# Kernel tuning notes

Hardware: AMD Instinct MI355X
Metric: run time of the kernel (lower is better)

## Reference

```python
import jax, jax.numpy as jnp
import numpy as np
from jax import lax

LOG2PI = float(np.log(2.0 * np.pi))
N_K, N_T, N_C, N_D, N_SPK = 256, 128, 32, 10, 1000000

def _std_normal_logpdf(x):
    return -0.5 * (x * x + LOG2PI)

def _normal_logpdf(x, mu, log_sig):
    z = (x - mu) * jnp.exp(-log_sig)
    return -0.5 * (z * z + LOG2PI) - log_sig

def safe_log(x, minval=1e-10):
    return jnp.log(x + minval)

def setup_inputs() -> dict:
    key = jax.random.key(0)
    ks_ = jax.random.split(key, 8)
    s = jax.random.normal(ks_[0], (N_SPK, N_D), dtype=jnp.float32)
    y = jax.random.normal(ks_[1], (N_K, N_T), dtype=jnp.float32)
    ks = jax.random.randint(ks_[2], (N_SPK,), 0, N_K, dtype=jnp.int32)
    ts = jax.random.randint(ks_[3], (N_SPK,), 0, N_T, dtype=jnp.int32)
    means = jax.random.normal(ks_[4], (N_C, N_D), dtype=jnp.float32)
    A = jax.random.normal(ks_[5], (N_C, N_D, N_D), dtype=jnp.float32)
    covs = jnp.einsum('cij,ckj->cik', A, A) / N_D + jnp.eye(N_D, dtype=jnp.float32)
    b_mu = jax.random.normal(ks_[6], (N_C,), dtype=jnp.float32)
    b_log_sig = jax.random.normal(ks_[7], (N_C,), dtype=jnp.float32)
    beta_mu = jax.random.normal(jax.random.fold_in(key, 10), (N_C, N_T), dtype=jnp.float32)
    beta_log_sig = jax.random.normal(jax.random.fold_in(key, 11), (N_C, N_T), dtype=jnp.float32)
    return {"s": s, "y": y, "ks": ks, "ts": ts, "means": means, "covs": covs,
            "b_mu": b_mu, "b_log_sig": b_log_sig, "beta_mu": beta_mu, "beta_log_sig": beta_log_sig}

def _mvn_ll(s, means, covs):
    # ll[n, c] = MVN(means[c], covs[c]).log_prob(s[n]); loop over small n_c via lax.map
    L = jnp.linalg.cholesky(covs)                       # (c, d, d)
    logdet = 2.0 * jnp.sum(jnp.log(jnp.diagonal(L, axis1=1, axis2=2)), axis=1)  # (c,)
    d = s.shape[1]
    def comp(args):
        mu, Lc, ld = args
        diff = s - mu                                   # (n, d)
        z = jax.scipy.linalg.solve_triangular(Lc, diff.T, lower=True)  # (d, n)
        return -0.5 * (d * LOG2PI + ld + jnp.sum(z * z, axis=0))       # (n,)
    return lax.map(comp, (means, L, logdet)).T          # (n, c)

def reference(s, y, ks, ts, means, covs, b_mu, b_log_sig, beta_mu, beta_log_sig):
    # sampling=False path: use variational means
    b_sample, beta_sample = b_mu, beta_mu               # (c,), (c, t)
    # log_lambdas[k, c, t] = b[c] + beta[c, t] * y[k, t]
    log_lambdas = b_sample[None, :, None] + beta_sample[None, :, :] * y[:, None, :]
    log_pis = jax.nn.log_softmax(log_lambdas, axis=1)   # (k, c, t)
    ll = _mvn_ll(s, means, covs)                        # (n, c)
    logits = ll + log_pis[ks, :, ts]                    # per-spike gather -> (n, c)
    r = jax.nn.softmax(logits, axis=1)                  # responsibilities (n, c)
    log_prior = jnp.sum(_std_normal_logpdf(b_sample)) + jnp.sum(_std_normal_logpdf(beta_sample))
    log_q = jnp.sum(_normal_logpdf(b_sample, b_mu, b_log_sig)) + \
            jnp.sum(_normal_logpdf(beta_sample, beta_mu, beta_log_sig))
    elbo = log_prior - log_q
    elbo += jnp.sum(r * logits)
    elbo -= jnp.sum(r * safe_log(r))
    return elbo
```

## Files before the change

kernel.cpp:

```cpp
#include <hip/hip_runtime.h>
#include <hip/hip_bf16.h>
#include <math.h>

#define NK 256
#define NT 128
#define NC 32
#define ND 10
#define NSPK 1000000
#define LOG2PI 1.8378770664093453f
#define NCHUNK ((NSPK + 255) / 256)
#define GRID 1024

#define FSTR 36
#define LDS_DW (256 * FSTR)

typedef __attribute__((ext_vector_type(8))) short short8;
typedef __attribute__((ext_vector_type(4))) float floatx4;
typedef __attribute__((ext_vector_type(4))) int intx4;

union FragCvt { intx4 i; short8 s; };


__device__ inline unsigned pack_bf16(float a, float b) {
  __hip_bfloat16 ha = __float2bfloat16(a), hb = __float2bfloat16(b);
  unsigned short ua, ub;
  __builtin_memcpy(&ua, &ha, 2);
  __builtin_memcpy(&ub, &hb, 2);
  return (unsigned)ua | ((unsigned)ub << 16);
}

__global__ void prep_kernel(const float* __restrict__ y,
                            const float* __restrict__ means,
                            const float* __restrict__ covs,
                            const float* __restrict__ b_mu,
                            const float* __restrict__ b_ls,
                            const float* __restrict__ beta_mu,
                            const float* __restrict__ beta_ls,
                            int* __restrict__ wt,
                            float* __restrict__ cpack,
                            float* __restrict__ pisT,
                            double* __restrict__ acc,
                            unsigned int* __restrict__ counter) {
  int blk = blockIdx.x;
  int tid = threadIdx.x;

  if (blk == 0) {
    int c = tid;
    if (c >= NC) return;

    float M[ND][ND];
    #pragma unroll
    for (int i = 0; i < ND; ++i)
      #pragma unroll
      for (int j = 0; j < ND; ++j)
        M[i][j] = covs[c * ND * ND + i * ND + j];

    float logdet = 0.f;
    #pragma unroll
    for (int j = 0; j < ND; ++j) {
      float d = M[j][j];
      #pragma unroll
      for (int k = 0; k < ND; ++k) if (k < j) d -= M[j][k] * M[j][k];
      float sq = sqrtf(d);
      M[j][j] = sq;
      logdet += 2.f * __logf(sq);
      float inv = 1.f / sq;
      #pragma unroll
      for (int i = 0; i < ND; ++i) {
        if (i > j) {
          float s2 = M[i][j];
          #pragma unroll
          for (int k = 0; k < ND; ++k) if (k < j) s2 -= M[i][k] * M[j][k];
          M[i][j] = s2 * inv;
        }
      }
    }

    #pragma unroll
    for (int j = 0; j < ND; ++j) {
      M[j][j] = 1.f / M[j][j];
      #pragma unroll
      for (int i = 0; i < ND; ++i) {
        if (i > j) {
          float s2 = 0.f;
          #pragma unroll
          for (int k = 0; k < ND; ++k) if (k >= j && k < i) s2 += M[i][k] * M[k][j];
          M[i][j] = -s2 / M[i][i];
        }
      }
    }

    float pd[ND];
    #pragma unroll
    for (int i = 0; i < ND; ++i) {
      #pragma unroll
      for (int jj = 0; jj < ND; ++jj) {
        if (jj >= i) {
          float s2 = 0.f;
          #pragma unroll
          for (int k = 0; k < ND; ++k) if (k >= jj) s2 += M[k][i] * M[k][jj];
          if (jj > i) M[i][jj] = s2;
          else pd[i] = s2;
        }
      }
    }

    float mu[ND], q[ND];
    #pragma unroll
    for (int i = 0; i < ND; ++i) mu[i] = means[c * ND + i];
    float muPmu = 0.f;
    #pragma unroll
    for (int i = 0; i < ND; ++i) {
      float a2 = pd[i] * mu[i];
      #pragma unroll
      for (int j = 0; j < ND; ++j) {
        if (j < i) a2 += M[j][i] * mu[j];
        if (j > i) a2 += M[i][j] * mu[j];
      }
      q[i] = a2;
      muPmu += mu[i] * a2;
    }
    float cst = -0.5f * ((float)ND * LOG2PI + logdet + muPmu);

    float wv[64];
    int p = 0;
    #pragma unroll
    for (int i = 0; i < ND; ++i)
      #pragma unroll
      for (int j = 0; j < ND; ++j)
        if (j >= i && !(i == 9 && j == 9))
          wv[p++] = (i == j) ? -0.5f * pd[i] : -M[i][j];
    #pragma unroll
    for (int i = 0; i < ND; ++i) wv[54 + i] = q[i];

    #pragma unroll
    for (int j = 0; j < 32; ++j) {
      float a = wv[2 * j], b = wv[2 * j + 1];
      float ah = __bfloat162float(__float2bfloat16(a));
      float bh = __bfloat162float(__float2bfloat16(b));
      wt[c * 32 + j] = (int)pack_bf16(ah, bh);
      wt[(32 + c) * 32 + j] = (int)pack_bf16(a - ah, b - bh);
    }
    cpack[c] = cst;
    cpack[32 + c] = -0.5f * pd[9];

  } else if (blk == 1) {
    float local = 0.f;
    for (int i = tid; i < NC; i += 256)
      local += fmaf(-0.5f * b_mu[i], b_mu[i], b_ls[i]);
    for (int i = tid; i < NC * NT; i += 256)
      local += fmaf(-0.5f * beta_mu[i], beta_mu[i], beta_ls[i]);
    #pragma unroll
    for (int off = 32; off > 0; off >>= 1) local += __shfl_down(local, off);
    __shared__ float red[4];
    if ((tid & 63) == 0) red[tid >> 6] = local;
    __syncthreads();
    if (tid == 0) {
      acc[0] = (double)(red[0] + red[1] + red[2] + red[3]);
      counter[0] = 0u;
    }

  } else {
    int id = (blk - 2) * 256 + tid;
    int t = id & (NT - 1);
    float yv = y[id];
    float v[NC];
    float m = -1e30f;
    #pragma unroll
    for (int c = 0; c < NC; ++c) {
      v[c] = fmaf(beta_mu[c * NT + t], yv, b_mu[c]);
      m = fmaxf(m, v[c]);
    }
    float ssum = 0.f;
    #pragma unroll
    for (int c = 0; c < NC; ++c) ssum += __expf(v[c] - m);
    float lz = m + __logf(ssum);
    float* outp = pisT + (size_t)id * NC;
    #pragma unroll
    for (int c = 0; c < NC; ++c) outp[c] = v[c] - lz;
  }
}

__global__ __launch_bounds__(256, 4)
void spike_kernel(const float* __restrict__ s,
                  const int* __restrict__ ks,
                  const int* __restrict__ ts,
                  const int* __restrict__ wt,
                  const float* __restrict__ cpack,
                  const float* __restrict__ pisT,
                  double* __restrict__ acc,
                  unsigned int* __restrict__ counter,
                  float* __restrict__ out) {
  __shared__ int lds[LDS_DW];
  __shared__ float red[4];

  int tid = threadIdx.x;
  int wv_ = tid >> 6, L = tid & 63;
  int r = L & 15, q = L >> 4;

  FragCvt bf[2][2][2];
  #pragma unroll
  for (int h = 0; h < 2; ++h)
    #pragma unroll
    for (int nt = 0; nt < 2; ++nt)
      #pragma unroll
      for (int ks2 = 0; ks2 < 2; ++ks2)
        bf[h][nt][ks2].i =
            *(const intx4*)&wt[(h * 32 + nt * 16 + r) * 32 + ks2 * 16 + q * 4];

  float lse_sum = 0.f;

  for (int ci = blockIdx.x; ci < NCHUNK; ci += GRID) {
    int n = ci * 256 + tid;
    int nc = n < NSPK ? n : (NSPK - 1);

    const float2* srow = (const float2*)(s + (size_t)nc * ND);
    float sv[ND];
    #pragma unroll
    for (int i = 0; i < 5; ++i) {
      float2 v2 = srow[i];
      sv[2 * i] = v2.x;
      sv[2 * i + 1] = v2.y;
    }
    int kk_ = ks[nc], tt_ = ts[nc];

    float fv[64];
    {
      int p = 0;
      #pragma unroll
      for (int i = 0; i < ND; ++i)
        #pragma unroll
        for (int j = 0; j < ND; ++j)
          if (j >= i && !(i == 9 && j == 9)) fv[p++] = sv[i] * sv[j];
      #pragma unroll
      for (int i = 0; i < ND; ++i) fv[54 + i] = sv[i];
    }

    __syncthreads();
    {
      int rb = tid * FSTR;
      #pragma unroll
      for (int ch = 0; ch < 8; ++ch) {
        intx4 v;
        v.x = (int)pack_bf16(fv[8 * ch + 0], fv[8 * ch + 1]);
        v.y = (int)pack_bf16(fv[8 * ch + 2], fv[8 * ch + 3]);
        v.z = (int)pack_bf16(fv[8 * ch + 4], fv[8 * ch + 5]);
        v.w = (int)pack_bf16(fv[8 * ch + 6], fv[8 * ch + 7]);
        *(intx4*)&lds[rb + ch * 4] = v;
      }
    }
    __syncthreads();

    floatx4 accf[4][2];
    #pragma unroll
    for (int mt = 0; mt < 4; ++mt)
      #pragma unroll
      for (int nt = 0; nt < 2; ++nt)
        accf[mt][nt] = (floatx4){0.f, 0.f, 0.f, 0.f};

    #pragma unroll
    for (int mt = 0; mt < 4; ++mt) {
      #pragma unroll
      for (int ks2 = 0; ks2 < 2; ++ks2) {
        FragCvt a;
        a.i = *(const intx4*)&lds[(wv_ * 64 + mt * 16 + r) * FSTR + ks2 * 16 + q * 4];
        #pragma unroll
        for (int nt = 0; nt < 2; ++nt) {
          accf[mt][nt] = __builtin_amdgcn_mfma_f32_16x16x32_bf16(
              a.s, bf[0][nt][ks2].s, accf[mt][nt], 0, 0, 0);
          accf[mt][nt] = __builtin_amdgcn_mfma_f32_16x16x32_bf16(
              a.s, bf[1][nt][ks2].s, accf[mt][nt], 0, 0, 0);
        }
      }
    }

    const float4* lpp = (const float4*)(pisT + (size_t)(kk_ * NT + tt_) * NC);
    float4 lpv[8];
    #pragma unroll
    for (int i = 0; i < 8; ++i) lpv[i] = lpp[i];

    __syncthreads();

    #pragma unroll
    for (int mt = 0; mt < 4; ++mt)
      #pragma unroll
      for (int nt = 0; nt < 2; ++nt)
        #pragma unroll
        for (int rr = 0; rr < 4; ++rr) {
          int srow_ = wv_ * 64 + mt * 16 + q * 4 + rr;
          lds[srow_ * FSTR + nt * 16 + r] = __float_as_int(accf[mt][nt][rr]);
        }
    __syncthreads();

    {
      float lp[32];
      #pragma unroll
      for (int i = 0; i < 8; ++i) {
        lp[4 * i + 0] = lpv[i].x; lp[4 * i + 1] = lpv[i].y;
        lp[4 * i + 2] = lpv[i].z; lp[4 * i + 3] = lpv[i].w;
      }
      float s9sq = sv[9] * sv[9];
      int base = tid * FSTR;
      float lg[32];
      #pragma unroll
      for (int g = 0; g < 8; ++g) {
        intx4 lv = *(const intx4*)&lds[base + g * 4];
        lg[4 * g + 0] = __int_as_float(lv.x);
        lg[4 * g + 1] = __int_as_float(lv.y);
        lg[4 * g + 2] = __int_as_float(lv.z);
        lg[4 * g + 3] = __int_as_float(lv.w);
      }
      #pragma unroll
      for (int c = 0; c < 32; ++c)
        lg[c] += lp[c] + fmaf(cpack[32 + c], s9sq, cpack[c]);

      float m = lg[0];
      #pragma unroll
      for (int c = 1; c < 32; ++c) m = fmaxf(m, lg[c]);
      float ssum = 0.f;
      #pragma unroll
      for (int c = 0; c < 32; ++c) ssum += __expf(lg[c] - m);
      if (n < NSPK) lse_sum += m + __logf(ssum);
    }
  }

  #pragma unroll
  for (int off = 32; off > 0; off >>= 1) lse_sum += __shfl_down(lse_sum, off);
  if ((tid & 63) == 0) red[tid >> 6] = lse_sum;
  __syncthreads();
  if (tid == 0) {
    atomicAdd(acc, (double)(red[0] + red[1] + red[2] + red[3]));
    __threadfence();
    unsigned int old = atomicAdd(counter, 1u);
    if (old == GRID - 1) {
      __threadfence();
      double v = atomicAdd(acc, 0.0);
      out[0] = (float)v;
    }
  }
}

extern "C" void kernel_launch(void* const* d_in, const int* in_sizes, int n_in,
                              void* d_out, int out_size, void* d_ws, size_t ws_size,
                              hipStream_t stream) {
  const float* s       = (const float*)d_in[0];
  const float* y       = (const float*)d_in[1];
  const int*   ks      = (const int*)d_in[2];
  const int*   ts      = (const int*)d_in[3];
  const float* means   = (const float*)d_in[4];
  const float* covs    = (const float*)d_in[5];
  const float* b_mu    = (const float*)d_in[6];
  const float* b_ls    = (const float*)d_in[7];
  const float* beta_mu = (const float*)d_in[8];
  const float* beta_ls = (const float*)d_in[9];
  float* out = (float*)d_out;

  char* ws = (char*)d_ws;
  double* acc           = (double*)ws;
  unsigned int* counter = (unsigned int*)(ws + 8);
  float* cpack          = (float*)(ws + 64);
  int* wt               = (int*)(ws + 1024);
  float* pisT           = (float*)(ws + 16384);

  prep_kernel<<<2 + (NK * NT) / 256, 256, 0, stream>>>(
      y, means, covs, b_mu, b_ls, beta_mu, beta_ls, wt, cpack, pisT, acc, counter);
  spike_kernel<<<GRID, 256, 0, stream>>>(
      s, ks, ts, wt, cpack, pisT, acc, counter, out);
}
```

Baseline: 168.0 us.

## Prefetch next chunk, use dynamic atomic work queue, store log-pis in fp16

The fixed grid-stride loop becomes an atomic work queue, and the next chunk's spike features and gather index are prefetched during the current chunk's MFMA and softmax. The log-pi table is stored as fp16, halving the gather traffic, and feature packing streams into LDS in groups of eight instead of holding a 64-float array. This aims to hide global load latency and balance load across blocks. In exchange it lowers the precision of log_pis, holds more registers live, and adds an atomic per chunk.

```diff
diff --git a/kernel.cpp b/kernel.cpp
--- a/kernel.cpp
+++ b/kernel.cpp
@@ -1,5 +1,6 @@
 #include <hip/hip_runtime.h>
 #include <hip/hip_bf16.h>
+#include <hip/hip_fp16.h>
 #include <math.h>
 
 #define NK 256
@@ -19,6 +20,7 @@
 typedef __attribute__((ext_vector_type(4))) int intx4;
 
 union FragCvt { intx4 i; short8 s; };
+union H2Cvt { int i; __half2 h; };
 
 
 __device__ inline unsigned pack_bf16(float a, float b) {
@@ -38,9 +40,10 @@
                             const float* __restrict__ beta_ls,
                             int* __restrict__ wt,
                             float* __restrict__ cpack,
-                            float* __restrict__ pisT,
+                            __half* __restrict__ pisT,
                             double* __restrict__ acc,
-                            unsigned int* __restrict__ counter) {
+                            unsigned int* __restrict__ counter,
+                            unsigned int* __restrict__ queue) {
   int blk = blockIdx.x;
   int tid = threadIdx.x;
 
@@ -158,6 +161,7 @@
     if (tid == 0) {
       acc[0] = (double)(red[0] + red[1] + red[2] + red[3]);
       counter[0] = 0u;
+      queue[0] = GRID;
     }
 
   } else {
@@ -175,24 +179,27 @@
     #pragma unroll
     for (int c = 0; c < NC; ++c) ssum += __expf(v[c] - m);
     float lz = m + __logf(ssum);
-    float* outp = pisT + (size_t)id * NC;
-    #pragma unroll
-    for (int c = 0; c < NC; ++c) outp[c] = v[c] - lz;
+    __half* outp = pisT + (size_t)id * NC;
+    #pragma unroll
+    for (int c = 0; c < NC; ++c) outp[c] = __float2half(v[c] - lz);
   }
 }
 
-__global__ __launch_bounds__(256, 4)
-void spike_kernel(const float* __restrict__ s,
-                  const int* __restrict__ ks,
-                  const int* __restrict__ ts,
-                  const int* __restrict__ wt,
-                  const float* __restrict__ cpack,
-                  const float* __restrict__ pisT,
-                  double* __restrict__ acc,
-                  unsigned int* __restrict__ counter,
-                  float* __restrict__ out) {
+__global__ void __launch_bounds__(256)
+__attribute__((amdgpu_waves_per_eu(4, 4)))
+spike_kernel(const float* __restrict__ s,
+             const int* __restrict__ ks,
+             const int* __restrict__ ts,
+             const int* __restrict__ wt,
+             const float* __restrict__ cpack,
+             const __half* __restrict__ pisT,
+             double* __restrict__ acc,
+             unsigned int* __restrict__ counter,
+             unsigned int* __restrict__ queue,
+             float* __restrict__ out) {
   __shared__ int lds[LDS_DW];
   __shared__ float red[4];
+  __shared__ int nextc_sh;
 
   int tid = threadIdx.x;
   int wv_ = tid >> 6, L = tid & 63;
@@ -210,46 +217,84 @@
 
   float lse_sum = 0.f;
 
-  for (int ci = blockIdx.x; ci < NCHUNK; ci += GRID) {
-    int n = ci * 256 + tid;
+  int chunk = blockIdx.x;
+  float svc[ND];
+  int ktc;
+  {
+    int n = chunk * 256 + tid;
     int nc = n < NSPK ? n : (NSPK - 1);
-
     const float2* srow = (const float2*)(s + (size_t)nc * ND);
-    float sv[ND];
     #pragma unroll
     for (int i = 0; i < 5; ++i) {
       float2 v2 = srow[i];
-      sv[2 * i] = v2.x;
-      sv[2 * i + 1] = v2.y;
-    }
-    int kk_ = ks[nc], tt_ = ts[nc];
-
-    float fv[64];
-    {
-      int p = 0;
-      #pragma unroll
-      for (int i = 0; i < ND; ++i)
-        #pragma unroll
-        for (int j = 0; j < ND; ++j)
-          if (j >= i && !(i == 9 && j == 9)) fv[p++] = sv[i] * sv[j];
-      #pragma unroll
-      for (int i = 0; i < ND; ++i) fv[54 + i] = sv[i];
-    }
+      svc[2 * i] = v2.x;
+      svc[2 * i + 1] = v2.y;
+    }
+    ktc = ks[nc] * NT + ts[nc];
+  }
+
+  while (chunk < NCHUNK) {
+    int ncur = chunk * 256 + tid;
 
     __syncthreads();
+
     {
       int rb = tid * FSTR;
-      #pragma unroll
-      for (int ch = 0; ch < 8; ++ch) {
-        intx4 v;
-        v.x = (int)pack_bf16(fv[8 * ch + 0], fv[8 * ch + 1]);
-        v.y = (int)pack_bf16(fv[8 * ch + 2], fv[8 * ch + 3]);
-        v.z = (int)pack_bf16(fv[8 * ch + 4], fv[8 * ch + 5]);
-        v.w = (int)pack_bf16(fv[8 * ch + 6], fv[8 * ch + 7]);
-        *(intx4*)&lds[rb + ch * 4] = v;
-      }
-    }
+      float f[8];
+      int p = 0;
+      #pragma unroll
+      for (int i = 0; i < ND; ++i) {
+        #pragma unroll
+        for (int j = i; j < ND; ++j) {
+          if (i == 9 && j == 9) continue;
+          f[p & 7] = svc[i] * svc[j];
+          if ((p & 7) == 7) {
+            intx4 v;
+            v.x = (int)pack_bf16(f[0], f[1]);
+            v.y = (int)pack_bf16(f[2], f[3]);
+            v.z = (int)pack_bf16(f[4], f[5]);
+            v.w = (int)pack_bf16(f[6], f[7]);
+            *(intx4*)&lds[rb + (p >> 3) * 4] = v;
+          }
+          ++p;
+        }
+      }
+      #pragma unroll
+      for (int i = 0; i < ND; ++i) {
+        f[p & 7] = svc[i];
+        if ((p & 7) == 7) {
+          intx4 v;
+          v.x = (int)pack_bf16(f[0], f[1]);
+          v.y = (int)pack_bf16(f[2], f[3]);
+          v.z = (int)pack_bf16(f[4], f[5]);
+          v.w = (int)pack_bf16(f[6], f[7]);
+          *(intx4*)&lds[rb + (p >> 3) * 4] = v;
+        }
+        ++p;
+      }
+    }
+
+    if (tid == 0) nextc_sh = (int)atomicAdd(queue, 1u);
+
     __syncthreads();
+
+    int nextc = nextc_sh;
+
+    float svn[ND];
+    int ktn;
+    {
+      int cc = nextc < NCHUNK ? nextc : (NCHUNK - 1);
+      int n = cc * 256 + tid;
+      int nc = n < NSPK ? n : (NSPK - 1);
+      const float2* srow = (const float2*)(s + (size_t)nc * ND);
+      #pragma unroll
+      for (int i = 0; i < 5; ++i) {
+        float2 v2 = srow[i];
+        svn[2 * i] = v2.x;
+        svn[2 * i + 1] = v2.y;
+      }
+      ktn = ks[nc] * NT + ts[nc];
+    }
 
     floatx4 accf[4][2];
     #pragma unroll
@@ -274,11 +319,6 @@
       }
     }
 
-    const float4* lpp = (const float4*)(pisT + (size_t)(kk_ * NT + tt_) * NC);
-    float4 lpv[8];
-    #pragma unroll
-    for (int i = 0; i < 8; ++i) lpv[i] = lpp[i];
-
     __syncthreads();
 
     #pragma unroll
@@ -293,13 +333,12 @@
     __syncthreads();
 
     {
-      float lp[32];
-      #pragma unroll
-      for (int i = 0; i < 8; ++i) {
-        lp[4 * i + 0] = lpv[i].x; lp[4 * i + 1] = lpv[i].y;
-        lp[4 * i + 2] = lpv[i].z; lp[4 * i + 3] = lpv[i].w;
-      }
-      float s9sq = sv[9] * sv[9];
+      const intx4* lpp = (const intx4*)(pisT + (size_t)ktc * NC);
+      intx4 lraw[4];
+      #pragma unroll
+      for (int i = 0; i < 4; ++i) lraw[i] = lpp[i];
+
+      float s9sq = svc[9] * svc[9];
       int base = tid * FSTR;
       float lg[32];
       #pragma unroll
@@ -311,8 +350,13 @@
         lg[4 * g + 3] = __int_as_float(lv.w);
       }
       #pragma unroll
-      for (int c = 0; c < 32; ++c)
-        lg[c] += lp[c] + fmaf(cpack[32 + c], s9sq, cpack[c]);
+      for (int g = 0; g < 16; ++g) {
+        H2Cvt hc;
+        hc.i = ((const int*)lraw)[g];
+        float lo = __low2float(hc.h), hi = __high2float(hc.h);
+        lg[2 * g + 0] += lo + fmaf(cpack[32 + 2 * g + 0], s9sq, cpack[2 * g + 0]);
+        lg[2 * g + 1] += hi + fmaf(cpack[32 + 2 * g + 1], s9sq, cpack[2 * g + 1]);
+      }
 
       float m = lg[0];
       #pragma unroll
@@ -320,8 +364,13 @@
       float ssum = 0.f;
       #pragma unroll
       for (int c = 0; c < 32; ++c) ssum += __expf(lg[c] - m);
-      if (n < NSPK) lse_sum += m + __logf(ssum);
-    }
+      if (ncur < NSPK) lse_sum += m + __logf(ssum);
+    }
+
+    chunk = nextc;
+    ktc = ktn;
+    #pragma unroll
+    for (int i = 0; i < ND; ++i) svc[i] = svn[i];
   }
 
   #pragma unroll
@@ -358,12 +407,14 @@
   char* ws = (char*)d_ws;
   double* acc           = (double*)ws;
   unsigned int* counter = (unsigned int*)(ws + 8);
+  unsigned int* queue   = (unsigned int*)(ws + 12);
   float* cpack          = (float*)(ws + 64);
   int* wt               = (int*)(ws + 1024);
-  float* pisT           = (float*)(ws + 16384);
+  __half* pisT          = (__half*)(ws + 16384);
 
   prep_kernel<<<2 + (NK * NT) / 256, 256, 0, stream>>>(
-      y, means, covs, b_mu, b_ls, beta_mu, beta_ls, wt, cpack, pisT, acc, counter);
+      y, means, covs, b_mu, b_ls, beta_mu, beta_ls, wt, cpack, pisT, acc,
+      counter, queue);
   spike_kernel<<<GRID, 256, 0, stream>>>(
-      s, ks, ts, wt, cpack, pisT, acc, counter, out);
+      s, ks, ts, wt, cpack, pisT, acc, counter, queue, out);
 }
```

Result: no change. 169.0 us (+0.6%).
